# Performance work log

Hardware: AMD Instinct MI355X
Metric: run time of the kernel (lower is better)

Reference implementation:

```python
import jax, jax.numpy as jnp
import numpy as np

N = 50000
IN_DIM = 128
HID = 16
HEADS = 8
NUM_CLASSES = 16
NEG_SLOPE = 0.2


def _glorot(key, shape):
    fan_in, fan_out = shape[0], shape[-1]
    lim = float(np.sqrt(6.0 / (fan_in + fan_out)))
    return jax.random.uniform(key, shape, jnp.float32, -lim, lim)


def setup_inputs() -> dict:
    key = jax.random.key(0)
    ks = jax.random.split(key, 12)
    x = jax.random.normal(ks[0], (N, IN_DIM), jnp.float32)
    edge_index = jax.random.randint(ks[1], (2, 1600000), 0, N, jnp.int64)
    # conv1: in=IN_DIM, out per head=HID, heads=HEADS
    Wl1 = _glorot(ks[2], (IN_DIM, HEADS * HID))
    Wr1 = _glorot(ks[3], (IN_DIM, HEADS * HID))
    att1 = _glorot(ks[4], (HEADS, HID))
    b1 = jnp.zeros((HEADS * HID,), jnp.float32)
    # conv2: in=HID*HEADS, out per head=NUM_CLASSES
    Wl2 = _glorot(ks[5], (HEADS * HID, HEADS * NUM_CLASSES))
    Wr2 = _glorot(ks[6], (HEADS * HID, HEADS * NUM_CLASSES))
    att2 = _glorot(ks[7], (HEADS, NUM_CLASSES))
    b2 = jnp.zeros((HEADS * NUM_CLASSES,), jnp.float32)
    # final linear: NUM_CLASSES*HEADS -> NUM_CLASSES
    Wlin = _glorot(ks[8], (HEADS * NUM_CLASSES, NUM_CLASSES))
    blin = jnp.zeros((NUM_CLASSES,), jnp.float32)
    return dict(x=x, edge_index=edge_index, Wl1=Wl1, Wr1=Wr1, att1=att1, b1=b1,
                Wl2=Wl2, Wr2=Wr2, att2=att2, b2=b2, Wlin=Wlin, blin=blin)


def _gatv2_conv(x, src, dst, Wl, Wr, att, bias, heads, out_ch):
    n = x.shape[0]
    xl = (x @ Wl).reshape(n, heads, out_ch)  # source transform
    xr = (x @ Wr).reshape(n, heads, out_ch)  # target transform
    # additive attention logits per edge (GATv2)
    e = jax.nn.leaky_relu(xl[src] + xr[dst], NEG_SLOPE)          # [E,H,C]
    logits = jnp.einsum('ehc,hc->eh', e, att)                     # [E,H]
    # per-destination segment softmax
    m = jax.ops.segment_max(logits, dst, num_segments=n)          # [N,H]
    a = jnp.exp(logits - m[dst])                                  # [E,H]
    s = jax.ops.segment_sum(a, dst, num_segments=n)               # [N,H]
    alpha = a / (s[dst] + 1e-16)
    out = jax.ops.segment_sum(alpha[:, :, None] * xl[src], dst, num_segments=n)
    return out.reshape(n, heads * out_ch) + bias


def reference(x, edge_index, Wl1, Wr1, att1, b1, Wl2, Wr2, att2, b2, Wlin, blin):
    n = x.shape[0]
    # add self-loops (PyG GATv2Conv default add_self_loops=True)
    loop = jnp.arange(n, dtype=edge_index.dtype)
    src = jnp.concatenate([edge_index[0], loop])
    dst = jnp.concatenate([edge_index[1], loop])
    h = _gatv2_conv(x, src, dst, Wl1, Wr1, att1, b1, HEADS, HID)
    h = jax.nn.relu(h)  # dropout identity in eval mode
    h = _gatv2_conv(h, src, dst, Wl2, Wr2, att2, b2, HEADS, NUM_CLASSES)
    h = jax.nn.relu(h)
    logits = h @ Wlin + blin
    return jax.nn.log_softmax(logits, axis=1)
```

## Files before the change

### kernel.cpp

```cpp
#include <hip/hip_runtime.h>

#define HEADS 8
#define FDIM 128
#define NCLS 16
#define NEG_SLOPE 0.2f
#define LOG2E 1.4426950408889634f

typedef __attribute__((ext_vector_type(8))) short bf16x8;
typedef __attribute__((ext_vector_type(4))) float f32x4;

__device__ __forceinline__ unsigned short f2bf(float f) {
    unsigned u = __float_as_uint(f);
    unsigned r = u + 0x7FFFu + ((u >> 16) & 1u);
    return (unsigned short)(r >> 16);
}

__global__ __launch_bounds__(256) void gemm_csr(const float* __restrict__ Xf,
                                                const unsigned short* __restrict__ Xb,
                                                const float* __restrict__ W0,
                                                const float* __restrict__ W1,
                                                unsigned short* __restrict__ Y0,
                                                unsigned short* __restrict__ Y1,
                                                int n,
                                                const int* __restrict__ srcs,
                                                const int* __restrict__ dsts,
                                                int* __restrict__ cnt,
                                                int* __restrict__ adj,
                                                int E0, int pad, int GB, int SB) {
    __shared__ __align__(16) unsigned short ws[8 * 4 * 64 * 8];
    const int t = threadIdx.x;
    const int x = blockIdx.x;
    int gIdx;
    if (SB > 0) {
        if ((x % 5) == 4) {
            int i = (x / 5) * 256 + t;
            const int stride = SB * 256;
            for (; i < E0; i += stride) {
                const int d = dsts[i];
                const int rk = atomicAdd(&cnt[d], 1);
                if (rk < pad) adj[(size_t)d * pad + rk] = srcs[i];
            }
            return;
        }
        gIdx = (x / 5) * 4 + (x % 5);
    } else {
        gIdx = x;
    }
    const int side = (gIdx >= GB) ? 1 : 0;
    const float* W = side ? W1 : W0;
    unsigned short* Y = side ? Y1 : Y0;
    const int bid = side ? gIdx - GB : gIdx;

#pragma unroll
    for (int i = 0; i < 16; i++) {
        const int f = t + i * 256;
        const int k = f >> 5, n4 = f & 31;
        const float4 v = *(const float4*)(W + k * 128 + n4 * 4);
        const int kc = k >> 5, q = (k >> 3) & 3, j = k & 7;
        const float vv[4] = {v.x, v.y, v.z, v.w};
#pragma unroll
        for (int e = 0; e < 4; e++) {
            const int nn = n4 * 4 + e;
            ws[((((nn >> 4) * 4 + kc) * 64 + q * 16 + (nn & 15)) << 3) + j] = f2bf(vv[e]);
        }
    }
    __syncthreads();

    const int w = t >> 6, lane = t & 63;
    const int q = lane >> 4, m = lane & 15;
    const bf16x8* wb = (const bf16x8*)ws;
    const int Gh = (n + 63) >> 6;

    for (int tile = bid; tile < Gh; tile += GB) {
        const int nb = tile * 64;
        const int arow = nb + w * 16 + m;
        bf16x8 af[4];
        if (arow < n) {
            if (Xb) {
                const unsigned short* xp = Xb + (size_t)arow * 128 + q * 8;
#pragma unroll
                for (int kc = 0; kc < 4; kc++) af[kc] = *(const bf16x8*)(xp + kc * 32);
            } else {
                const float* xp = Xf + (size_t)arow * 128 + q * 8;
#pragma unroll
                for (int kc = 0; kc < 4; kc++) {
                    const float4 v0 = *(const float4*)(xp + kc * 32);
                    const float4 v1 = *(const float4*)(xp + kc * 32 + 4);
                    union { unsigned short us[8]; bf16x8 b; } pk;
                    pk.us[0] = f2bf(v0.x); pk.us[1] = f2bf(v0.y);
                    pk.us[2] = f2bf(v0.z); pk.us[3] = f2bf(v0.w);
                    pk.us[4] = f2bf(v1.x); pk.us[5] = f2bf(v1.y);
                    pk.us[6] = f2bf(v1.z); pk.us[7] = f2bf(v1.w);
                    af[kc] = pk.b;
                }
            }
        } else {
#pragma unroll
            for (int kc = 0; kc < 4; kc++) af[kc] = (bf16x8){0,0,0,0,0,0,0,0};
        }
        f32x4 acc[8];
#pragma unroll
        for (int i = 0; i < 8; i++) acc[i] = (f32x4){0.f, 0.f, 0.f, 0.f};
#pragma unroll
        for (int kc = 0; kc < 4; kc++) {
#pragma unroll
            for (int ct = 0; ct < 8; ct++)
                acc[ct] = __builtin_amdgcn_mfma_f32_16x16x32_bf16(
                    af[kc], wb[(ct * 4 + kc) * 64 + lane], acc[ct], 0, 0, 0);
        }
#pragma unroll
        for (int ct = 0; ct < 8; ct++) {
#pragma unroll
            for (int r = 0; r < 4; r++) {
                const int row = nb + w * 16 + q * 4 + r;
                if (row < n) Y[(size_t)row * 128 + ct * 16 + m] = f2bf(acc[ct][r]);
            }
        }
    }
}

#define GATHER_EDGE4(SRC, GATE)                                              \
    {                                                                        \
        const uint4 lv_ = *(const uint4*)(xl + (size_t)(SRC) * FDIM + col);  \
        const float l0_ = __uint_as_float(lv_.x << 16);                      \
        const float l1_ = __uint_as_float(lv_.x & 0xFFFF0000u);              \
        const float l2_ = __uint_as_float(lv_.y << 16);                      \
        const float l3_ = __uint_as_float(lv_.y & 0xFFFF0000u);              \
        const float l4_ = __uint_as_float(lv_.z << 16);                      \
        const float l5_ = __uint_as_float(lv_.z & 0xFFFF0000u);              \
        const float l6_ = __uint_as_float(lv_.w << 16);                      \
        const float l7_ = __uint_as_float(lv_.w & 0xFFFF0000u);              \
        float z_, p_;                                                        \
        z_ = l0_ + r0; z_ = fmaxf(z_, NEG_SLOPE * z_); p_  = z_ * a0;        \
        z_ = l1_ + r1; z_ = fmaxf(z_, NEG_SLOPE * z_); p_ += z_ * a1;        \
        z_ = l2_ + r2; z_ = fmaxf(z_, NEG_SLOPE * z_); p_ += z_ * a2;        \
        z_ = l3_ + r3; z_ = fmaxf(z_, NEG_SLOPE * z_); p_ += z_ * a3;        \
        z_ = l4_ + r4; z_ = fmaxf(z_, NEG_SLOPE * z_); p_ += z_ * a4;        \
        z_ = l5_ + r5; z_ = fmaxf(z_, NEG_SLOPE * z_); p_ += z_ * a5;        \
        z_ = l6_ + r6; z_ = fmaxf(z_, NEG_SLOPE * z_); p_ += z_ * a6;        \
        z_ = l7_ + r7; z_ = fmaxf(z_, NEG_SLOPE * z_); p_ += z_ * a7;        \
        p_ += __shfl_xor(p_, 1, 64);                                         \
        const float e_ = exp2f(p_ - mx) * (GATE);                            \
        s += e_;                                                             \
        c0 += e_ * l0_; c1 += e_ * l1_; c2 += e_ * l2_; c3 += e_ * l3_;      \
        c4 += e_ * l4_; c5 += e_ * l5_; c6 += e_ * l6_; c7 += e_ * l7_;      \
    }

template <bool HEAD>
__global__ __launch_bounds__(256) void node_gather(const unsigned short* __restrict__ xl,
                                                   const unsigned short* __restrict__ xr,
                                                   const float* __restrict__ att,
                                                   const int* __restrict__ adj,
                                                   const int* __restrict__ cnt,
                                                   const float* __restrict__ bias,
                                                   unsigned short* __restrict__ outC,
                                                   const float* __restrict__ headW,
                                                   const float* __restrict__ headB,
                                                   float* __restrict__ outH,
                                                   int n, int pad) {
    __shared__ float WsL[HEAD ? FDIM * NCLS : 1];
    __shared__ __align__(16) float stage[HEAD ? 4 : 1][FDIM];
    const int t = threadIdx.x;
    if (HEAD) {
        for (int i = t; i < FDIM * NCLS; i += 256) WsL[i] = headW[i];
        __syncthreads();
    }
    const int lane = t & 63;
    const int w = t >> 6;
    const int node = blockIdx.x * 4 + w;
    if (node >= n) return;
    const int g = lane >> 4;
    const int sub = lane & 15;
    const int col = sub * 8;
    float a0, a1, a2, a3, a4, a5, a6, a7;
    {
        const float4 v0 = *(const float4*)(att + col);
        const float4 v1 = *(const float4*)(att + col + 4);
        a0 = v0.x * LOG2E; a1 = v0.y * LOG2E; a2 = v0.z * LOG2E; a3 = v0.w * LOG2E;
        a4 = v1.x * LOG2E; a5 = v1.y * LOG2E; a6 = v1.z * LOG2E; a7 = v1.w * LOG2E;
    }
    float r0, r1, r2, r3, r4, r5, r6, r7;
    float sl0, sl1, sl2, sl3, sl4, sl5, sl6, sl7;
    {
        const uint4 rv = *(const uint4*)(xr + (size_t)node * FDIM + col);
        r0 = __uint_as_float(rv.x << 16); r1 = __uint_as_float(rv.x & 0xFFFF0000u);
        r2 = __uint_as_float(rv.y << 16); r3 = __uint_as_float(rv.y & 0xFFFF0000u);
        r4 = __uint_as_float(rv.z << 16); r5 = __uint_as_float(rv.z & 0xFFFF0000u);
        r6 = __uint_as_float(rv.w << 16); r7 = __uint_as_float(rv.w & 0xFFFF0000u);
        const uint4 lv = *(const uint4*)(xl + (size_t)node * FDIM + col);
        sl0 = __uint_as_float(lv.x << 16); sl1 = __uint_as_float(lv.x & 0xFFFF0000u);
        sl2 = __uint_as_float(lv.y << 16); sl3 = __uint_as_float(lv.y & 0xFFFF0000u);
        sl4 = __uint_as_float(lv.z << 16); sl5 = __uint_as_float(lv.z & 0xFFFF0000u);
        sl6 = __uint_as_float(lv.w << 16); sl7 = __uint_as_float(lv.w & 0xFFFF0000u);
    }
    float mx;
    {
        float z, p;
        z = sl0 + r0; z = fmaxf(z, NEG_SLOPE * z); p  = z * a0;
        z = sl1 + r1; z = fmaxf(z, NEG_SLOPE * z); p += z * a1;
        z = sl2 + r2; z = fmaxf(z, NEG_SLOPE * z); p += z * a2;
        z = sl3 + r3; z = fmaxf(z, NEG_SLOPE * z); p += z * a3;
        z = sl4 + r4; z = fmaxf(z, NEG_SLOPE * z); p += z * a4;
        z = sl5 + r5; z = fmaxf(z, NEG_SLOPE * z); p += z * a5;
        z = sl6 + r6; z = fmaxf(z, NEG_SLOPE * z); p += z * a6;
        z = sl7 + r7; z = fmaxf(z, NEG_SLOPE * z); p += z * a7;
        p += __shfl_xor(p, 1, 64);
        mx = p;
    }
    float s, c0, c1, c2, c3, c4, c5, c6, c7;
    if (g == 0) { s = 1.f; c0 = sl0; c1 = sl1; c2 = sl2; c3 = sl3;
                  c4 = sl4; c5 = sl5; c6 = sl6; c7 = sl7; }
    else        { s = 0.f; c0 = c1 = c2 = c3 = c4 = c5 = c6 = c7 = 0.f; }

    const int* ap = adj + (size_t)node * pad;
    const int deg = min(cnt[node], pad);
    int j = 0;
    for (; j + 8 <= deg; j += 8) {
        const int e0 = ap[j + g];
        const int e1 = ap[j + 4 + g];
        GATHER_EDGE4(e0, 1.f)
        GATHER_EDGE4(e1, 1.f)
    }
    for (; j < deg; j += 4) {
        const int idx = j + g;
        const int e0 = (idx < deg) ? ap[idx] : ap[deg - 1];
        const float gate = (idx < deg) ? 1.f : 0.f;
        GATHER_EDGE4(e0, gate)
    }
    s  += __shfl_xor(s, 16, 64);  s  += __shfl_xor(s, 32, 64);
    c0 += __shfl_xor(c0, 16, 64); c0 += __shfl_xor(c0, 32, 64);
    c1 += __shfl_xor(c1, 16, 64); c1 += __shfl_xor(c1, 32, 64);
    c2 += __shfl_xor(c2, 16, 64); c2 += __shfl_xor(c2, 32, 64);
    c3 += __shfl_xor(c3, 16, 64); c3 += __shfl_xor(c3, 32, 64);
    c4 += __shfl_xor(c4, 16, 64); c4 += __shfl_xor(c4, 32, 64);
    c5 += __shfl_xor(c5, 16, 64); c5 += __shfl_xor(c5, 32, 64);
    c6 += __shfl_xor(c6, 16, 64); c6 += __shfl_xor(c6, 32, 64);
    c7 += __shfl_xor(c7, 16, 64); c7 += __shfl_xor(c7, 32, 64);

    const float inv = 1.f / (s + 1e-16f);
    float o0, o1, o2, o3, o4, o5, o6, o7;
    {
        const float4 b0 = *(const float4*)(bias + col);
        const float4 b1 = *(const float4*)(bias + col + 4);
        o0 = fmaxf(c0 * inv + b0.x, 0.f); o1 = fmaxf(c1 * inv + b0.y, 0.f);
        o2 = fmaxf(c2 * inv + b0.z, 0.f); o3 = fmaxf(c3 * inv + b0.w, 0.f);
        o4 = fmaxf(c4 * inv + b1.x, 0.f); o5 = fmaxf(c5 * inv + b1.y, 0.f);
        o6 = fmaxf(c6 * inv + b1.z, 0.f); o7 = fmaxf(c7 * inv + b1.w, 0.f);
    }

    if (!HEAD) {
        if (g == 0) {
            union { unsigned short us[8]; uint4 u4; } pk;
            pk.us[0] = f2bf(o0); pk.us[1] = f2bf(o1);
            pk.us[2] = f2bf(o2); pk.us[3] = f2bf(o3);
            pk.us[4] = f2bf(o4); pk.us[5] = f2bf(o5);
            pk.us[6] = f2bf(o6); pk.us[7] = f2bf(o7);
            *(uint4*)(outC + (size_t)node * FDIM + col) = pk.u4;
        }
        return;
    }
    if (g == 0) {
        *(float4*)&stage[w][col]     = make_float4(o0, o1, o2, o3);
        *(float4*)&stage[w][col + 4] = make_float4(o4, o5, o6, o7);
    }
    const int cls = lane & 15;
    const int q = lane >> 4;
    float acc = 0.f;
#pragma unroll
    for (int k = 0; k < 32; k++)
        acc += stage[w][q * 32 + k] * WsL[(q * 32 + k) * NCLS + cls];
    acc += __shfl_xor(acc, 16, 64);
    acc += __shfl_xor(acc, 32, 64);
    acc += headB[cls];
    float m2 = acc;
    m2 = fmaxf(m2, __shfl_xor(m2, 8, 64));
    m2 = fmaxf(m2, __shfl_xor(m2, 4, 64));
    m2 = fmaxf(m2, __shfl_xor(m2, 2, 64));
    m2 = fmaxf(m2, __shfl_xor(m2, 1, 64));
    float sm = __expf(acc - m2);
    sm += __shfl_xor(sm, 8, 64);
    sm += __shfl_xor(sm, 4, 64);
    sm += __shfl_xor(sm, 2, 64);
    sm += __shfl_xor(sm, 1, 64);
    if (lane < 16)
        outH[(size_t)node * NCLS + cls] = acc - m2 - __logf(sm);
}

extern "C" void kernel_launch(void* const* d_in, const int* in_sizes, int n_in,
                              void* d_out, int out_size, void* d_ws, size_t ws_size,
                              hipStream_t stream) {
    const float* x    = (const float*)d_in[0];
    const int*   edge = (const int*)d_in[1];
    const float* Wl1  = (const float*)d_in[2];
    const float* Wr1  = (const float*)d_in[3];
    const float* att1 = (const float*)d_in[4];
    const float* b1   = (const float*)d_in[5];
    const float* Wl2  = (const float*)d_in[6];
    const float* Wr2  = (const float*)d_in[7];
    const float* att2 = (const float*)d_in[8];
    const float* b2   = (const float*)d_in[9];
    const float* Wlin = (const float*)d_in[10];
    const float* blin = (const float*)d_in[11];

    const int N = in_sizes[0] / FDIM;
    const int E0 = in_sizes[1] / 2;
    const int* srcs = edge;
    const int* dsts = edge + E0;

    int PAD = 96;
    {
        size_t need = (size_t)3 * N * FDIM * 2 + (size_t)N * 4 + (size_t)N * PAD * 4;
        if (need > ws_size) PAD = 72;
    }

    unsigned short* A = (unsigned short*)d_ws;
    unsigned short* B = A + (size_t)N * FDIM;
    unsigned short* C = B + (size_t)N * FDIM;
    int* cnt   = (int*)(C + (size_t)N * FDIM);
    int* adj   = cnt + N;

    const int GB = 512;
    const int SB = 256;
    const int node_blocks = (N + 3) / 4;

    hipMemsetAsync(cnt, 0, (size_t)N * sizeof(int), stream);

    gemm_csr<<<5 * SB, 256, 0, stream>>>(
        x, nullptr, Wl1, Wr1, A, B, N, srcs, dsts, cnt, adj, E0, PAD, GB, SB);
    node_gather<false><<<node_blocks, 256, 0, stream>>>(
        A, B, att1, adj, cnt, b1, C, nullptr, nullptr, nullptr, N, PAD);

    gemm_csr<<<2 * GB, 256, 0, stream>>>(
        nullptr, C, Wl2, Wr2, A, B, N, nullptr, nullptr, nullptr, nullptr, 0, PAD, GB, 0);
    node_gather<true><<<node_blocks, 256, 0, stream>>>(
        A, B, att2, adj, cnt, b2, nullptr, Wlin, blin, (float*)d_out, N, PAD);
}
```

Measured before the change: 361.9 us.

## Build CSR via two-pass bucketed scatter with 16-bit indices and swizzled LDS

Replaces the direct per-edge atomic scatter into the padded adjacency with a two-pass scheme. Edges are first binned into coarse destination buckets (256 nodes times 8 slots), then a separate kernel scatters each bucket into the padded per-node adjacency. The adjacency list now stores 16-bit source indices, which halves gather index traffic. The weight tile in LDS is XOR-swizzled to reduce bank conflicts. The risks are real: 16-bit indices only hold for N <= 65536, bucket overflow beyond BCAP silently drops edges, and the extra kernel launch and pass add cost.

```diff
diff --git a/kernel.cpp b/kernel.cpp
--- a/kernel.cpp
+++ b/kernel.cpp
@@ -5,6 +5,11 @@
 #define NCLS 16
 #define NEG_SLOPE 0.2f
 #define LOG2E 1.4426950408889634f
+
+#define BSHIFT 8
+#define NBUCK 196
+#define NSLOT 8
+#define BCAP 1280
 
 typedef __attribute__((ext_vector_type(8))) short bf16x8;
 typedef __attribute__((ext_vector_type(4))) float f32x4;
@@ -24,9 +29,9 @@
                                                 int n,
                                                 const int* __restrict__ srcs,
                                                 const int* __restrict__ dsts,
-                                                int* __restrict__ cnt,
-                                                int* __restrict__ adj,
-                                                int E0, int pad, int GB, int SB) {
+                                                unsigned* __restrict__ bucket,
+                                                int* __restrict__ bcnt,
+                                                int E0, int GB, int SB) {
     __shared__ __align__(16) unsigned short ws[8 * 4 * 64 * 8];
     const int t = threadIdx.x;
     const int x = blockIdx.x;
@@ -35,10 +40,14 @@
         if ((x % 5) == 4) {
             int i = (x / 5) * 256 + t;
             const int stride = SB * 256;
+            const int slot = x & 7;
             for (; i < E0; i += stride) {
+                const int s = srcs[i];
                 const int d = dsts[i];
-                const int rk = atomicAdd(&cnt[d], 1);
-                if (rk < pad) adj[(size_t)d * pad + rk] = srcs[i];
+                const int g = (d >> BSHIFT) * NSLOT + slot;
+                const unsigned v = ((unsigned)(d & 255) << 16) | (unsigned)s;
+                const int pos = atomicAdd(&bcnt[g], 1);
+                if (pos < BCAP) bucket[(size_t)g * BCAP + pos] = v;
             }
             return;
         }
@@ -57,11 +66,13 @@
         const int k = f >> 5, n4 = f & 31;
         const float4 v = *(const float4*)(W + k * 128 + n4 * 4);
         const int kc = k >> 5, q = (k >> 3) & 3, j = k & 7;
+        const int g3 = n4 >> 2;
         const float vv[4] = {v.x, v.y, v.z, v.w};
 #pragma unroll
         for (int e = 0; e < 4; e++) {
             const int nn = n4 * 4 + e;
-            ws[((((nn >> 4) * 4 + kc) * 64 + q * 16 + (nn & 15)) << 3) + j] = f2bf(vv[e]);
+            const int u = ((((nn >> 4) * 4 + kc) * 64 + q * 16 + (nn & 15)) ^ g3);
+            ws[(u << 3) + j] = f2bf(vv[e]);
         }
     }
     __syncthreads();
@@ -106,7 +117,7 @@
 #pragma unroll
             for (int ct = 0; ct < 8; ct++)
                 acc[ct] = __builtin_amdgcn_mfma_f32_16x16x32_bf16(
-                    af[kc], wb[(ct * 4 + kc) * 64 + lane], acc[ct], 0, 0, 0);
+                    af[kc], wb[(ct * 4 + kc) * 64 + (lane ^ ct)], acc[ct], 0, 0, 0);
         }
 #pragma unroll
         for (int ct = 0; ct < 8; ct++) {
@@ -116,6 +127,23 @@
                 if (row < n) Y[(size_t)row * 128 + ct * 16 + m] = f2bf(acc[ct][r]);
             }
         }
+    }
+}
+
+__global__ __launch_bounds__(256) void csr_scatter(const unsigned* __restrict__ bucket,
+                                                   const int* __restrict__ bcnt,
+                                                   int* __restrict__ cnt,
+                                                   unsigned short* __restrict__ adj,
+                                                   int pad) {
+    const int g = blockIdx.x;
+    const int base = (g / NSLOT) << BSHIFT;
+    const int cs = min(bcnt[g], BCAP);
+    const unsigned* bp = bucket + (size_t)g * BCAP;
+    for (int i = threadIdx.x; i < cs; i += 256) {
+        const unsigned v = bp[i];
+        const int d = base + (int)(v >> 16);
+        const int rk = atomicAdd(&cnt[d], 1);
+        if (rk < pad) adj[(size_t)d * pad + rk] = (unsigned short)(v & 0xFFFFu);
     }
 }
 
@@ -150,7 +178,7 @@
 __global__ __launch_bounds__(256) void node_gather(const unsigned short* __restrict__ xl,
                                                    const unsigned short* __restrict__ xr,
                                                    const float* __restrict__ att,
-                                                   const int* __restrict__ adj,
+                                                   const unsigned short* __restrict__ adj,
                                                    const int* __restrict__ cnt,
                                                    const float* __restrict__ bias,
                                                    unsigned short* __restrict__ outC,
@@ -212,18 +240,18 @@
                   c4 = sl4; c5 = sl5; c6 = sl6; c7 = sl7; }
     else        { s = 0.f; c0 = c1 = c2 = c3 = c4 = c5 = c6 = c7 = 0.f; }
 
-    const int* ap = adj + (size_t)node * pad;
+    const unsigned short* ap = adj + (size_t)node * pad;
     const int deg = min(cnt[node], pad);
     int j = 0;
     for (; j + 8 <= deg; j += 8) {
-        const int e0 = ap[j + g];
-        const int e1 = ap[j + 4 + g];
+        const int e0 = (int)ap[j + g];
+        const int e1 = (int)ap[j + 4 + g];
         GATHER_EDGE4(e0, 1.f)
         GATHER_EDGE4(e1, 1.f)
     }
     for (; j < deg; j += 4) {
         const int idx = j + g;
-        const int e0 = (idx < deg) ? ap[idx] : ap[deg - 1];
+        const int e0 = (idx < deg) ? (int)ap[idx] : (int)ap[deg - 1];
         const float gate = (idx < deg) ? 1.f : 0.f;
         GATHER_EDGE4(e0, gate)
     }
@@ -309,7 +337,8 @@
 
     int PAD = 96;
     {
-        size_t need = (size_t)3 * N * FDIM * 2 + (size_t)N * 4 + (size_t)N * PAD * 4;
+        size_t need = (size_t)3 * N * FDIM * 2 + (size_t)(N + NBUCK * NSLOT) * 4
+                    + (size_t)N * PAD * 2 + (size_t)NBUCK * NSLOT * BCAP * 4;
         if (need > ws_size) PAD = 72;
     }
 
@@ -317,21 +346,24 @@
     unsigned short* B = A + (size_t)N * FDIM;
     unsigned short* C = B + (size_t)N * FDIM;
     int* cnt   = (int*)(C + (size_t)N * FDIM);
-    int* adj   = cnt + N;
+    int* bcnt  = cnt + N;
+    unsigned short* adj = (unsigned short*)(bcnt + NBUCK * NSLOT);
+    unsigned* bucket = (unsigned*)(adj + (size_t)N * PAD);
 
     const int GB = 512;
     const int SB = 256;
     const int node_blocks = (N + 3) / 4;
 
-    hipMemsetAsync(cnt, 0, (size_t)N * sizeof(int), stream);
+    hipMemsetAsync(cnt, 0, (size_t)(N + NBUCK * NSLOT) * sizeof(int), stream);
 
     gemm_csr<<<5 * SB, 256, 0, stream>>>(
-        x, nullptr, Wl1, Wr1, A, B, N, srcs, dsts, cnt, adj, E0, PAD, GB, SB);
+        x, nullptr, Wl1, Wr1, A, B, N, srcs, dsts, bucket, bcnt, E0, GB, SB);
+    csr_scatter<<<NBUCK * NSLOT, 256, 0, stream>>>(bucket, bcnt, cnt, adj, PAD);
     node_gather<false><<<node_blocks, 256, 0, stream>>>(
         A, B, att1, adj, cnt, b1, C, nullptr, nullptr, nullptr, N, PAD);
 
     gemm_csr<<<2 * GB, 256, 0, stream>>>(
-        nullptr, C, Wl2, Wr2, A, B, N, nullptr, nullptr, nullptr, nullptr, 0, PAD, GB, 0);
+        nullptr, C, Wl2, Wr2, A, B, N, nullptr, nullptr, nullptr, nullptr, 0, GB, 0);
     node_gather<true><<<node_blocks, 256, 0, stream>>>(
         A, B, att2, adj, cnt, b2, nullptr, Wlin, blin, (float*)d_out, N, PAD);
 }
```

After: 582.5 us. +60.9%, slower.
